# Kernel optimization log

Measured on AMD Instinct MI355X. Metric: run time of the kernel, lower is better.

Reference implementation:

```python
import jax, jax.numpy as jnp
import numpy as np

D_MODEL = 1024
N_HEADS = 16
D_K = D_MODEL // N_HEADS
D_FF = 4096
B, S = 4, 2048
EPS = 1e-5


def layer_norm(x, gamma, beta):
    mu = jnp.mean(x, axis=-1, keepdims=True)
    var = jnp.var(x, axis=-1, keepdims=True)
    return (x - mu) * jax.lax.rsqrt(var + EPS) * gamma + beta


def setup_inputs() -> dict:
    key = jax.random.key(0)
    ks = jax.random.split(key, 16)
    s = 1.0 / np.sqrt(D_MODEL)
    inp = {
        "query": jax.random.normal(ks[0], (B, S, D_MODEL), jnp.float32),
        "key": jax.random.normal(ks[1], (B, S, D_MODEL), jnp.float32),
        "value": jax.random.normal(ks[2], (B, S, D_MODEL), jnp.float32),
        "mask": jnp.ones((B, S, S), jnp.int32),
        "Wq": jax.random.normal(ks[3], (D_MODEL, D_MODEL), jnp.float32) * s,
        "Wk": jax.random.normal(ks[4], (D_MODEL, D_MODEL), jnp.float32) * s,
        "Wv": jax.random.normal(ks[5], (D_MODEL, D_MODEL), jnp.float32) * s,
        "Wo": jax.random.normal(ks[6], (D_MODEL, D_MODEL), jnp.float32) * s,
        "bo": jnp.zeros((D_MODEL,), jnp.float32),
        "g1": jnp.ones((D_MODEL,), jnp.float32),
        "b1": jnp.zeros((D_MODEL,), jnp.float32),
        "g2": jnp.ones((D_MODEL,), jnp.float32),
        "b2": jnp.zeros((D_MODEL,), jnp.float32),
        "gff": jnp.ones((D_MODEL,), jnp.float32),
        "bff": jnp.zeros((D_MODEL,), jnp.float32),
        "W1": jax.random.normal(ks[7], (D_MODEL, D_FF), jnp.float32) * s,
        "bf1": jnp.zeros((D_FF,), jnp.float32),
        "W2": jax.random.normal(ks[8], (D_FF, D_MODEL), jnp.float32) / np.sqrt(D_FF),
        "bf2": jnp.zeros((D_MODEL,), jnp.float32),
    }
    return inp


def reference(query, key, value, mask, Wq, Wk, Wv, Wo, bo,
              g1, b1, g2, b2, gff, bff, W1, bf1, W2, bf2):
    # Multi-head attention (dropout = identity, eval mode)
    q = (query @ Wq.T).reshape(B, S, N_HEADS, D_K).transpose(0, 2, 1, 3)
    k = (key @ Wk.T).reshape(B, S, N_HEADS, D_K).transpose(0, 2, 1, 3)
    v = (value @ Wv.T).reshape(B, S, N_HEADS, D_K).transpose(0, 2, 1, 3)
    scores = jnp.einsum("bhqd,bhkd->bhqk", q, k) / np.sqrt(D_K)  # [B,H,S,S]
    scores = jnp.where(mask[:, None, :, :] == 0, jnp.float32(-1e9), scores)
    attn = jax.nn.softmax(scores, axis=-1)
    ctx = jnp.einsum("bhqk,bhkd->bhqd", attn, v)
    ctx = ctx.transpose(0, 2, 1, 3).reshape(B, S, D_MODEL)
    attn_out = ctx @ Wo.T + bo

    # residual + LN
    x = layer_norm(attn_out + query, g1, b1)

    # FeedForward (has its own internal LayerNorm)
    h = layer_norm(x, gff, bff)
    h = jax.nn.relu(h @ W1 + bf1)
    ff = h @ W2 + bf2

    return layer_norm(ff + x, g2, b2)
```

## Files before the change

### kernel.cpp

```cpp
#include <hip/hip_runtime.h>


#define DM   1024
#define DFF  4096
#define SEQ  2048

typedef unsigned short u16;
typedef short          sx8  __attribute__((ext_vector_type(8)));
typedef unsigned short ushx8 __attribute__((ext_vector_type(8)));
typedef unsigned short ushx4 __attribute__((ext_vector_type(4)));
typedef float          fx4  __attribute__((ext_vector_type(4)));
typedef unsigned int   ux2  __attribute__((ext_vector_type(2)));

__device__ __forceinline__ void async16(const void* g, void* l) {
  __builtin_amdgcn_global_load_lds((__attribute__((address_space(1))) void*)g,
                                   (__attribute__((address_space(3))) void*)l,
                                   16, 0, 0);
}
__device__ __forceinline__ float b2f(u16 u) {
  union { unsigned int i; float f; } v; v.i = ((unsigned int)u) << 16; return v.f;
}
__device__ __forceinline__ u16 f2b(float f) {
  union { float f; unsigned int i; } v; v.f = f;
  unsigned int r = v.i + 0x7fffu + ((v.i >> 16) & 1u);
  return (u16)(r >> 16);
}
__device__ __forceinline__ float fexp2(float x) {
#if __has_builtin(__builtin_amdgcn_exp2f)
  return __builtin_amdgcn_exp2f(x);
#else
  return exp2f(x);
#endif
}
__device__ __forceinline__ ushx8 ld8(const void* p, long idx, bool f32) {
  if (f32) {
    const float* s = (const float*)p + idx;
    fx4 a = *(const fx4*)s, b = *(const fx4*)(s + 4);
    ushx8 r;
    r[0] = f2b(a[0]); r[1] = f2b(a[1]); r[2] = f2b(a[2]); r[3] = f2b(a[3]);
    r[4] = f2b(b[0]); r[5] = f2b(b[1]); r[6] = f2b(b[2]); r[7] = f2b(b[3]);
    return r;
  }
  return *(const ushx8*)((const u16*)p + idx);
}
__device__ __forceinline__ void ld4f(const void* p, long idx, bool f32, float* o) {
  if (f32) {
    fx4 a = *(const fx4*)((const float*)p + idx);
    o[0] = a[0]; o[1] = a[1]; o[2] = a[2]; o[3] = a[3];
  } else {
    ushx4 a = *(const ushx4*)((const u16*)p + idx);
    o[0] = b2f(a[0]); o[1] = b2f(a[1]); o[2] = b2f(a[2]); o[3] = b2f(a[3]);
  }
}

__global__ void detect_kernel(const void* q, int* flags) {
  int lane = threadIdx.x;
  u16 v = ((const u16*)q)[lane << 1];
  int e = (v >> 7) & 0xff;
  int pl = (e >= 0x60 && e <= 0x8c) ? 1 : 0;
  unsigned long long m = __ballot(pl);
  if (lane == 0) { flags[0] = (__popcll(m) >= 40) ? 0 : 1; flags[1] = 0; flags[2] = 1; }
}

__global__ __launch_bounds__(256)
void mask_scan(const int* __restrict__ m, int* flags) {
  long i = (((long)blockIdx.x << 8) + threadIdx.x) << 3;
  const int4 a = *(const int4*)(m + i);
  const int4 b = *(const int4*)(m + i + 4);
  bool ok = a.x && a.y && a.z && a.w && b.x && b.y && b.z && b.w;
  if (!__all(ok)) { if ((threadIdx.x & 63) == 0) flags[2] = 0; }
}

__global__ __launch_bounds__(256)
void pack_w(const void* Wq, const void* Wk, const void* Wv, const void* Wo,
            u16* Wqkv, u16* Wo_bf, const int* f_p) {
  const bool f = (*f_p != 0);
  long i = (((long)blockIdx.x << 8) + threadIdx.x) << 3;
  const long QKVN = (long)3 * DM * DM;
  if (i < QKVN) {
    int row = (int)(i >> 10);
    const void* src = (row < DM) ? Wq : (row < 2 * DM ? Wk : Wv);
    long s = ((long)(row & (DM - 1)) << 10) + (i & 1023);
    *(ushx8*)(Wqkv + i) = ld8(src, s, f);
  } else {
    long j = i - QKVN;
    *(ushx8*)(Wo_bf + j) = ld8(Wo, j, f);
  }
}

__global__ __launch_bounds__(256)
void conv_bf3(const void* q, const void* k, const void* v, long off,
              u16* dst, long n, const int* f_p) {
  const bool f = (*f_p != 0);
  const void* src = (blockIdx.y == 0) ? q : (blockIdx.y == 1 ? k : v);
  long i = (((long)blockIdx.x << 8) + threadIdx.x) << 3;
  if (i < n) *(ushx8*)(dst + (long)blockIdx.y * n + i) = ld8(src, off + i, f);
}

template<bool RELU, bool BIAS, bool DBUF>
__global__ __launch_bounds__(256)
void gemm_bb(const u16* __restrict__ A, long az, const u16* __restrict__ B, long bz,
             const void* __restrict__ bias, u16* __restrict__ C, long cz,
             int M, int N, int K, int ldc, const int* biasf_p) {
  __shared__ __align__(16) u16 sA[(DBUF ? 2 : 1) * 128 * 64];
  __shared__ __align__(16) u16 sB[(DBUF ? 2 : 1) * 128 * 64];
  const int z = blockIdx.y;
  A += (long)z * az; B += (long)z * bz; C += (long)z * cz;
  const bool biasf = BIAS && (*biasf_p != 0);
  const int t = threadIdx.x;
  const int lane = t & 63, w = t >> 6;
  const int lm = lane & 15, lg = lane >> 4;
  const int ntil = N >> 7;
  const int bx = (blockIdx.x & 7) * ((int)gridDim.x >> 3) + (blockIdx.x >> 3);
  const int m0 = (bx / ntil) << 7;
  const int n0 = (bx % ntil) << 7;
  const int wm = (w & 1) << 6, wn = (w >> 1) << 6;

  fx4 acc[4][4];
#pragma unroll
  for (int i = 0; i < 4; ++i)
#pragma unroll
    for (int j = 0; j < 4; ++j) acc[i][j] = (fx4){0.f, 0.f, 0.f, 0.f};

  auto stage = [&](int so, int kt) {
#pragma unroll
    for (int it = 0; it < 4; ++it) {
      int ci = (it << 8) + t;
      int r = ci >> 3, cs = (ci & 7) ^ (r & 7);
      async16(&A[(size_t)(m0 + r) * K + kt + (cs << 3)], &sA[so + (ci << 3)]);
    }
#pragma unroll
    for (int it = 0; it < 4; ++it) {
      int ci = (it << 8) + t;
      int r = ci >> 3, cs = (ci & 7) ^ (r & 7);
      async16(&B[(size_t)(n0 + r) * K + kt + (cs << 3)], &sB[so + (ci << 3)]);
    }
  };

  auto compute = [&](int so) {
#pragma unroll
    for (int s = 0; s < 2; ++s) {
      const int g = (s << 2) + lg;
      sx8 afr[4], bfr[4];
#pragma unroll
      for (int i = 0; i < 4; ++i) {
        int ra = wm + (i << 4) + lm;
        afr[i] = *(const sx8*)&sA[so + ra * 64 + ((g ^ (ra & 7)) << 3)];
        int rb = wn + (i << 4) + lm;
        bfr[i] = *(const sx8*)&sB[so + rb * 64 + ((g ^ (rb & 7)) << 3)];
      }
      __builtin_amdgcn_s_setprio(1);
#pragma unroll
      for (int i = 0; i < 4; ++i)
#pragma unroll
        for (int j = 0; j < 4; ++j)
          acc[i][j] = __builtin_amdgcn_mfma_f32_16x16x32_bf16(afr[i], bfr[j], acc[i][j], 0, 0, 0);
      __builtin_amdgcn_s_setprio(0);
    }
  };

  if (DBUF) {
    const int NT = K >> 6;
    stage(0, 0);
    for (int n = 0; n < NT; ++n) {
      if (n + 1 < NT) {
        stage(((n + 1) & 1) << 13, (n + 1) << 6);
        asm volatile("s_waitcnt vmcnt(8)" ::: "memory");
      } else {
        asm volatile("s_waitcnt vmcnt(0)" ::: "memory");
      }
      __builtin_amdgcn_s_barrier();
      __builtin_amdgcn_sched_barrier(0);
      compute((n & 1) << 13);
      if (n + 1 < NT) __builtin_amdgcn_s_barrier();
    }
  } else {
    for (int kt = 0; kt < K; kt += 64) {
      __syncthreads();
      stage(0, kt);
      __syncthreads();
      compute(0);
    }
  }

#pragma unroll
  for (int j = 0; j < 4; ++j) {
    const int col = n0 + wn + (j << 4) + lm;
    float bv = 0.f;
    if (BIAS) bv = biasf ? ((const float*)bias)[col] : b2f(((const u16*)bias)[col]);
#pragma unroll
    for (int i = 0; i < 4; ++i) {
      const int row0 = m0 + wm + (i << 4) + (lg << 2);
#pragma unroll
      for (int r = 0; r < 4; ++r) {
        float v = acc[i][j][r] + bv;
        if (RELU) v = fmaxf(v, 0.f);
        C[(size_t)(row0 + r) * ldc + col] = f2b(v);
      }
    }
  }
}

template<bool RELU, bool BIAS>
__global__ __launch_bounds__(256)
void gemm_nt(const void* __restrict__ A, long aoff, const void* __restrict__ Bm,
             const void* __restrict__ bias, u16* __restrict__ C,
             int M, int N, int K,
             const int* af_p, const int* bf_p, const int* biasf_p) {
  __shared__ __align__(16) u16 sA[128 * 64];
  __shared__ __align__(16) u16 sB[128 * 64];
  const bool af = (*af_p != 0), bfl = (*bf_p != 0), biasf = (*biasf_p != 0);
  const int t = threadIdx.x;
  const int lane = t & 63, w = t >> 6;
  const int lm = lane & 15, lg = lane >> 4;
  const int ntil = N >> 7;
  const int m0 = (blockIdx.x / ntil) << 7;
  const int n0 = (blockIdx.x % ntil) << 7;
  const int wm = (w & 1) << 6, wn = (w >> 1) << 6;

  fx4 acc[4][4];
#pragma unroll
  for (int i = 0; i < 4; ++i)
#pragma unroll
    for (int j = 0; j < 4; ++j) acc[i][j] = (fx4){0.f, 0.f, 0.f, 0.f};

  for (int kt = 0; kt < K; kt += 64) {
    __syncthreads();
#pragma unroll
    for (int it = 0; it < 4; ++it) {
      int ci = (it << 8) + t;
      int r = ci >> 3, cs = (ci & 7) ^ (r & 7);
      ushx8 va = ld8(A, aoff + (long)(m0 + r) * K + kt + (cs << 3), af);
      *(ushx8*)&sA[ci << 3] = va;
      ushx8 vb = ld8(Bm, (long)(n0 + r) * K + kt + (cs << 3), bfl);
      *(ushx8*)&sB[ci << 3] = vb;
    }
    __syncthreads();
#pragma unroll
    for (int s = 0; s < 2; ++s) {
      const int g = (s << 2) + lg;
      sx8 afr[4], bfr[4];
#pragma unroll
      for (int i = 0; i < 4; ++i) {
        int ra = wm + (i << 4) + lm;
        afr[i] = *(const sx8*)&sA[ra * 64 + ((g ^ (ra & 7)) << 3)];
        int rb = wn + (i << 4) + lm;
        bfr[i] = *(const sx8*)&sB[rb * 64 + ((g ^ (rb & 7)) << 3)];
      }
#pragma unroll
      for (int i = 0; i < 4; ++i)
#pragma unroll
        for (int j = 0; j < 4; ++j)
          acc[i][j] = __builtin_amdgcn_mfma_f32_16x16x32_bf16(afr[i], bfr[j], acc[i][j], 0, 0, 0);
    }
  }

#pragma unroll
  for (int j = 0; j < 4; ++j) {
    const int col = n0 + wn + (j << 4) + lm;
    float bv = 0.f;
    if (BIAS) bv = biasf ? ((const float*)bias)[col] : b2f(((const u16*)bias)[col]);
#pragma unroll
    for (int i = 0; i < 4; ++i) {
      const int row0 = m0 + wm + (i << 4) + (lg << 2);
#pragma unroll
      for (int r = 0; r < 4; ++r) {
        float v = acc[i][j][r] + bv;
        if (RELU) v = fmaxf(v, 0.f);
        C[(size_t)(row0 + r) * N + col] = f2b(v);
      }
    }
  }
}

__global__ __launch_bounds__(256)
void transpose_any(const void* __restrict__ in, u16* __restrict__ out,
                   int R, int C, const int* f_p) {
  __shared__ u16 tile[64][68];
  const bool f = (*f_p != 0);
  const int r0 = blockIdx.y << 6, c0 = blockIdx.x << 6;
  const int t = threadIdx.x;
#pragma unroll
  for (int it = 0; it < 4; ++it) {
    int j = (it << 8) + t;
    int rr = j >> 4, cc4 = (j & 15) << 2;
    float v[4];
    ld4f(in, (long)(r0 + rr) * C + c0 + cc4, f, v);
#pragma unroll
    for (int q = 0; q < 4; ++q) tile[rr][cc4 + q] = f2b(v[q]);
  }
  __syncthreads();
#pragma unroll
  for (int it = 0; it < 4; ++it) {
    int j = (it << 8) + t;
    int cc = j >> 4, rr4 = (j & 15) << 2;
    ushx4 v;
    v[0] = tile[rr4 + 0][cc]; v[1] = tile[rr4 + 1][cc];
    v[2] = tile[rr4 + 2][cc]; v[3] = tile[rr4 + 3][cc];
    *(ushx4*)&out[(size_t)(c0 + cc) * R + r0 + rr4] = v;
  }
}

__global__ __launch_bounds__(256, 3)
void attn_kernel(const u16* __restrict__ qp, const u16* __restrict__ kp,
                 const u16* __restrict__ vp, int lds_,
                 const int* __restrict__ mask, u16* __restrict__ ctx,
                 const int* __restrict__ mflag) {
  __shared__ __align__(16) u16 smem[16384];
  u16* const sK  = smem;
  u16* const sVt = smem + 8192;
  unsigned* const sPal = (unsigned*)smem;

  const bool nomask = (*mflag != 0);
  const long boff = (long)blockIdx.y * SEQ * (long)lds_;
  qp += boff; kp += boff; vp += boff;
  mask += (size_t)blockIdx.y * ((size_t)SEQ * SEQ);
  ctx += (size_t)blockIdx.y * ((size_t)SEQ * DM);

  const int id = (blockIdx.x & 7) * ((int)gridDim.x >> 3) + (blockIdx.x >> 3);
  const int q0 = (id & 31) << 6;
  const int h  = id >> 5;
  const int t = threadIdx.x, lane = t & 63, w = t >> 6;
  const int hoff = h << 6;
  const int lm = lane & 15, lg = lane >> 4;
  const int myq = q0 + (w << 4) + lm;
  const int aslot = 20 * lg;

  const int kq = (t & 31) << 2, dg = (t >> 5) << 3;
  const int kg7 = (kq >> 3) & 7;
  const int k7o = kq & 7;
  const int vbrow = ((kq >> 6) << 6) + dg;
  unsigned* pw = sPal + (w << 10);
  const int wswz = (lm & 7) << 2;
  const int pwb = lm << 6;

  sx8 one_b;
#pragma unroll
  for (int j = 0; j < 8; ++j) one_b[j] = (short)0x3F80;

  sx8 aq[2];
#pragma unroll
  for (int s = 0; s < 2; ++s)
    aq[s] = *(const sx8*)&qp[(size_t)myq * lds_ + hoff + (((s << 2) + lg) << 3)];

  fx4 o[4];
#pragma unroll
  for (int i = 0; i < 4; ++i) o[i] = (fx4){0.f, 0.f, 0.f, 0.f};
  fx4 osum = (fx4){0.f, 0.f, 0.f, 0.f};
  float m_prev = -1e30f;
  const float SCL = 0.18033688f;
  const float RTHR = 44.36142f;

  const u16* vbase = vp + (size_t)kq * lds_ + hoff + dg;
  uint4 va = *(const uint4*)(vbase);
  uint4 vb_ = *(const uint4*)(vbase + (size_t)lds_);
  uint4 vc = *(const uint4*)(vbase + 2 * (size_t)lds_);
  uint4 vd = *(const uint4*)(vbase + 3 * (size_t)lds_);

  for (int kt = 0; kt < 16; ++kt) {
    const int k0 = kt << 7;
    __syncthreads();
#pragma unroll
    for (int it = 0; it < 4; ++it) {
      int ci = (it << 8) + t;
      int r = ci >> 3, cs = (ci & 7) ^ (r & 7);
      async16(&kp[(size_t)(k0 + r) * lds_ + hoff + (cs << 3)], &sK[ci << 3]);
    }
    {
      const unsigned A0[4] = {va.x, va.y, va.z, va.w};
      const unsigned B0[4] = {vb_.x, vb_.y, vb_.z, vb_.w};
      const unsigned C0[4] = {vc.x, vc.y, vc.z, vc.w};
      const unsigned D0[4] = {vd.x, vd.y, vd.z, vd.w};
#pragma unroll
      for (int j = 0; j < 8; ++j) {
        const unsigned sel = (j & 1) ? 0x07060302u : 0x05040100u;
        ux2 wv;
        wv[0] = __builtin_amdgcn_perm(B0[j >> 1], A0[j >> 1], sel);
        wv[1] = __builtin_amdgcn_perm(D0[j >> 1], C0[j >> 1], sel);
        *(ux2*)&sVt[(vbrow + j) * 64 + ((kg7 ^ j) << 3) + k7o] = wv;
      }
    }
    __syncthreads();

    if (kt + 1 < 16) {
      const u16* vn = vbase + (size_t)(k0 + 128) * lds_;
      va = *(const uint4*)(vn);
      vb_ = *(const uint4*)(vn + (size_t)lds_);
      vc = *(const uint4*)(vn + 2 * (size_t)lds_);
      vd = *(const uint4*)(vn + 3 * (size_t)lds_);
    }

    fx4 sc[8];
#pragma unroll
    for (int nt = 0; nt < 8; ++nt) sc[nt] = (fx4){0.f, 0.f, 0.f, 0.f};
    __builtin_amdgcn_s_setprio(1);
#pragma unroll
    for (int s = 0; s < 2; ++s) {
      const int g = (s << 2) + lg;
#pragma unroll
      for (int nt = 0; nt < 8; ++nt) {
        int rk = (nt << 4) + lm;
        sx8 bk = *(const sx8*)&sK[rk * 64 + ((g ^ (rk & 7)) << 3)];
        sc[nt] = __builtin_amdgcn_mfma_f32_16x16x32_bf16(bk, aq[s], sc[nt], 0, 0, 0);
      }
    }
    __builtin_amdgcn_s_setprio(0);

    if (!nomask) {
#pragma unroll
      for (int nt = 0; nt < 8; ++nt)
#pragma unroll
        for (int r = 0; r < 4; ++r) {
          const int col = k0 + (nt << 4) + (lg << 2) + r;
          if (mask[((size_t)myq << 11) + col] == 0) sc[nt][r] = -1e9f;
        }
    }

    float tm = sc[0][0];
#pragma unroll
    for (int nt = 0; nt < 8; ++nt)
#pragma unroll
      for (int r = 0; r < 4; ++r) tm = fmaxf(tm, sc[nt][r]);
    tm = fmaxf(tm, __shfl_xor(tm, 16));
    tm = fmaxf(tm, __shfl_xor(tm, 32));

    if (!__all(tm <= m_prev + RTHR)) {
      const float mn = fmaxf(m_prev, tm);
      const float alpha = fexp2((m_prev - mn) * SCL);
#pragma unroll
      for (int r = 0; r < 4; ++r) {
        float ar = __shfl(alpha, aslot + r);
#pragma unroll
        for (int ot = 0; ot < 4; ++ot) o[ot][r] *= ar;
        osum[r] *= ar;
      }
      m_prev = mn;
    }

    const float msc = m_prev * SCL;
    float pvv[8][4];
#pragma unroll
    for (int nt = 0; nt < 8; ++nt)
#pragma unroll
      for (int r = 0; r < 4; ++r)
        pvv[nt][r] = fexp2(__builtin_fmaf(sc[nt][r], SCL, -msc));

    unsigned cpk[8][2];
#pragma unroll
    for (int nt = 0; nt < 8; ++nt) {
      asm("v_cvt_pk_bf16_f32 %0, %1, %2" : "=v"(cpk[nt][0]) : "v"(pvv[nt][0]), "v"(pvv[nt][1]));
      asm("v_cvt_pk_bf16_f32 %0, %1, %2" : "=v"(cpk[nt][1]) : "v"(pvv[nt][2]), "v"(pvv[nt][3]));
    }

    __builtin_amdgcn_sched_barrier(0);
    __builtin_amdgcn_s_barrier();
    __builtin_amdgcn_sched_barrier(0);

#pragma unroll
    for (int nt = 0; nt < 8; ++nt)
      *(ux2*)&pw[pwb + (((nt << 3) + (lg << 1)) ^ wswz)] = (ux2){cpk[nt][0], cpk[nt][1]};

    __builtin_amdgcn_s_setprio(1);
#pragma unroll
    for (int ks = 0; ks < 4; ++ks) {
      sx8 ap = *(const sx8*)&pw[pwb + (((ks << 4) + (lg << 2)) ^ wswz)];
      const int vrow = ((ks >> 1) << 6);
      const int vgr = (((ks & 1) << 2) + lg) ^ (lm & 7);
#pragma unroll
      for (int ot = 0; ot < 4; ++ot) {
        sx8 bv = *(const sx8*)&sVt[(vrow + (ot << 4) + lm) * 64 + (vgr << 3)];
        o[ot] = __builtin_amdgcn_mfma_f32_16x16x32_bf16(ap, bv, o[ot], 0, 0, 0);
      }
      osum = __builtin_amdgcn_mfma_f32_16x16x32_bf16(ap, one_b, osum, 0, 0, 0);
    }
    __builtin_amdgcn_s_setprio(0);
  }

#pragma unroll
  for (int r = 0; r < 4; ++r) {
    const float ir = (osum[r] > 0.f) ? 1.f / osum[r] : 0.f;
#pragma unroll
    for (int ot = 0; ot < 4; ++ot) {
      const int rowg = q0 + (w << 4) + (lg << 2) + r;
      const int col = hoff + (ot << 4) + lm;
      ctx[((size_t)rowg << 10) + col] = f2b(o[ot][r] * ir);
    }
  }
}

__global__ __launch_bounds__(256)
void ln_dual(const u16* __restrict__ a, const void* __restrict__ res, long roff,
             const void* __restrict__ g1, const void* __restrict__ b1,
             const void* __restrict__ gf, const void* __restrict__ bf,
             u16* __restrict__ xo, u16* __restrict__ xlo, const int* f_p) {
  __shared__ float red[8];
  const bool f = (*f_p != 0);
  const int row = blockIdx.x, t = threadIdx.x;
  const int lane = t & 63, w = t >> 6;
  const size_t base = (size_t)row << 10;
  const int c = t << 2;

  ushx4 a4 = *(const ushx4*)(a + base + c);
  float rv[4];
  ld4f(res, roff + (long)base + c, f, rv);
  float v[4], s = 0.f, ss = 0.f;
#pragma unroll
  for (int j = 0; j < 4; ++j) { v[j] = b2f(a4[j]) + rv[j]; s += v[j]; ss += v[j] * v[j]; }
#pragma unroll
  for (int off = 32; off > 0; off >>= 1) { s += __shfl_xor(s, off); ss += __shfl_xor(ss, off); }
  if (lane == 0) { red[w] = s; red[4 + w] = ss; }
  __syncthreads();
  s = red[0] + red[1] + red[2] + red[3];
  ss = red[4] + red[5] + red[6] + red[7];
  float mu = s * (1.f / 1024.f);
  float rstd = rsqrtf(fmaxf(ss * (1.f / 1024.f) - mu * mu, 0.f) + 1e-5f);

  float g4[4], b4[4];
  ld4f(g1, c, f, g4); ld4f(b1, c, f, b4);
  float x[4], s2 = 0.f, ss2 = 0.f;
  ushx4 xo4;
#pragma unroll
  for (int j = 0; j < 4; ++j) {
    x[j] = (v[j] - mu) * rstd * g4[j] + b4[j];
    xo4[j] = f2b(x[j]);
    s2 += x[j]; ss2 += x[j] * x[j];
  }
  *(ushx4*)(xo + base + c) = xo4;
#pragma unroll
  for (int off = 32; off > 0; off >>= 1) { s2 += __shfl_xor(s2, off); ss2 += __shfl_xor(ss2, off); }
  __syncthreads();
  if (lane == 0) { red[w] = s2; red[4 + w] = ss2; }
  __syncthreads();
  s2 = red[0] + red[1] + red[2] + red[3];
  ss2 = red[4] + red[5] + red[6] + red[7];
  float mu2 = s2 * (1.f / 1024.f);
  float rstd2 = rsqrtf(fmaxf(ss2 * (1.f / 1024.f) - mu2 * mu2, 0.f) + 1e-5f);

  ld4f(gf, c, f, g4); ld4f(bf, c, f, b4);
  ushx4 xl4;
#pragma unroll
  for (int j = 0; j < 4; ++j)
    xl4[j] = f2b((x[j] - mu2) * rstd2 * g4[j] + b4[j]);
  *(ushx4*)(xlo + base + c) = xl4;
}

__global__ __launch_bounds__(256)
void ln_final(const u16* __restrict__ a, const u16* __restrict__ resx,
              const void* __restrict__ g, const void* __restrict__ bb,
              void* __restrict__ out, long ooff, const int* f_p) {
  __shared__ float red[8];
  const bool f = (*f_p != 0);
  const int row = blockIdx.x, t = threadIdx.x;
  const int lane = t & 63, w = t >> 6;
  const size_t base = (size_t)row << 10;
  const int c = t << 2;

  ushx4 a4 = *(const ushx4*)(a + base + c);
  ushx4 r4 = *(const ushx4*)(resx + base + c);
  float v[4], s = 0.f, ss = 0.f;
#pragma unroll
  for (int j = 0; j < 4; ++j) { v[j] = b2f(a4[j]) + b2f(r4[j]); s += v[j]; ss += v[j] * v[j]; }
#pragma unroll
  for (int off = 32; off > 0; off >>= 1) { s += __shfl_xor(s, off); ss += __shfl_xor(ss, off); }
  if (lane == 0) { red[w] = s; red[4 + w] = ss; }
  __syncthreads();
  s = red[0] + red[1] + red[2] + red[3];
  ss = red[4] + red[5] + red[6] + red[7];
  float mu = s * (1.f / 1024.f);
  float rstd = rsqrtf(fmaxf(ss * (1.f / 1024.f) - mu * mu, 0.f) + 1e-5f);

  float g4[4], b4[4];
  ld4f(g, c, f, g4); ld4f(bb, c, f, b4);
  if (f) {
    fx4 o4;
#pragma unroll
    for (int j = 0; j < 4; ++j) o4[j] = (v[j] - mu) * rstd * g4[j] + b4[j];
    *(fx4*)((float*)out + ooff + base + c) = o4;
  } else {
    ushx4 o4;
#pragma unroll
    for (int j = 0; j < 4; ++j) o4[j] = f2b((v[j] - mu) * rstd * g4[j] + b4[j]);
    *(ushx4*)((u16*)out + ooff + base + c) = o4;
  }
}

extern "C" void kernel_launch(void* const* d_in, const int* in_sizes, int n_in,
                              void* d_out, int out_size, void* d_ws, size_t ws_size,
                              hipStream_t stream) {
  (void)in_sizes; (void)n_in; (void)out_size;
  const void* query = d_in[0];
  const void* keyi  = d_in[1];
  const void* value = d_in[2];
  const int*  mask  = (const int*)d_in[3];
  const void* Wq = d_in[4];
  const void* Wk = d_in[5];
  const void* Wv = d_in[6];
  const void* Wo = d_in[7];
  const void* bo = d_in[8];
  const void* g1 = d_in[9];
  const void* b1 = d_in[10];
  const void* g2 = d_in[11];
  const void* b2 = d_in[12];
  const void* gff = d_in[13];
  const void* bff = d_in[14];
  const void* W1 = d_in[15];
  const void* bf1 = d_in[16];
  const void* W2 = d_in[17];
  const void* bf2 = d_in[18];

  char* p = (char*)d_ws;
  int* flags = (int*)p;
  const int* F = flags;
  const int* Z = flags + 1;
  const int* M = flags + 2;
  dim3 blk(256);

  const size_t FIXED = 4096 + ((size_t)24 << 20);
  const size_t needC = FIXED + (size_t)8192 * 14336;
  const size_t needA = FIXED + (size_t)4096 * 14336;
  const size_t needB = FIXED + (size_t)2048 * 14336;

  if (ws_size >= needB) {
    const int CH = (ws_size >= needC) ? 8192 : (ws_size >= needA) ? 4096 : 2048;
    const int nch = 8192 / CH;

    u16* Wqkv  = (u16*)(p + 4096);
    u16* Wo_bf = Wqkv + (size_t)3 * DM * DM;
    u16* W1T   = Wo_bf + (size_t)DM * DM;
    u16* W2T   = W1T + (size_t)DFF * DM;
    u16* D0    = W2T + (size_t)DM * DFF;
    u16* D1    = D0 + (size_t)3 * CH * DM;
    u16* D2    = D1 + (size_t)3 * CH * DM;
    u16* qb = D0;
    u16* qkv = D1;
    u16* ao = D1, *x = D1 + (size_t)CH * DM, *xln = D1 + (size_t)2 * CH * DM;
    u16* h = D0;
    u16* ctx = D2, *ff = D2;

    detect_kernel<<<1, 64, 0, stream>>>(query, flags);
    mask_scan<<<dim3(8192), blk, 0, stream>>>(mask, flags);
    pack_w<<<dim3(2048), blk, 0, stream>>>(Wq, Wk, Wv, Wo, Wqkv, Wo_bf, F);
    transpose_any<<<dim3(DFF / 64, DM / 64), blk, 0, stream>>>(W1, W1T, DM, DFF, F);
    transpose_any<<<dim3(DM / 64, DFF / 64), blk, 0, stream>>>(W2, W2T, DFF, DM, F);

    for (int c = 0; c < nch; ++c) {
      const long off = (long)c * CH * DM;
      const long n = (long)CH * DM;
      conv_bf3<<<dim3((int)(n >> 11), 3), blk, 0, stream>>>(query, keyi, value, off, qb, n, F);

      gemm_bb<false, false, false><<<dim3((CH / 128) * 8, 3), blk, 0, stream>>>(
          qb, (long)CH * DM, Wqkv, (long)DM * DM, nullptr,
          qkv, 1024L, CH, DM, DM, 3072, Z);

      const int bpc = CH / SEQ, b0 = c * bpc;
      attn_kernel<<<dim3(512, bpc), blk, 0, stream>>>(
          qkv, qkv + 1024, qkv + 2048, 3072,
          mask + (size_t)b0 * SEQ * SEQ, ctx, M);

      gemm_bb<false, true, true><<<dim3((CH / 128) * 8, 1), blk, 0, stream>>>(
          ctx, 0, Wo_bf, 0, bo, ao, 0, CH, DM, DM, DM, F);

      ln_dual<<<dim3(CH), blk, 0, stream>>>(ao, query, off, g1, b1, gff, bff, x, xln, F);

      gemm_bb<true, true, false><<<dim3((CH / 128) * 32, 1), blk, 0, stream>>>(
          xln, 0, W1T, 0, bf1, h, 0, CH, DFF, DM, DFF, F);
      gemm_bb<false, true, true><<<dim3((CH / 128) * 8, 1), blk, 0, stream>>>(
          h, 0, W2T, 0, bf2, ff, 0, CH, DM, DFF, DM, F);

      ln_final<<<dim3(CH), blk, 0, stream>>>(ff, x, g2, b2, d_out, off, F);
    }
  } else {
    const int CH = 2048, FH = 1024;
    const int nch = 8192 / CH;
    const size_t h0 = 4096;
    u16* W1T = (u16*)(p + h0);
    u16* W2T = W1T + (size_t)DFF * DM;
    u16* hb  = (u16*)(p + h0 + ((size_t)16 << 20));
    const size_t HB = (size_t)FH * DFF * 2;
    u16* r0 = (u16*)(p + h0 + ((size_t)16 << 20) + HB);
    const size_t CE = (size_t)CH * DM;
    u16* qp = r0;
    u16* kp = qp + CE;
    u16* vp = kp + CE;
    u16* ctxb = vp + CE;
    u16* x = qp; u16* xln = kp; u16* ao = vp; u16* ff = ctxb;

    detect_kernel<<<1, 64, 0, stream>>>(query, flags);
    mask_scan<<<dim3(8192), blk, 0, stream>>>(mask, flags);
    transpose_any<<<dim3(DFF / 64, DM / 64), blk, 0, stream>>>(W1, W1T, DM, DFF, F);
    transpose_any<<<dim3(DM / 64, DFF / 64), blk, 0, stream>>>(W2, W2T, DFF, DM, F);

    for (int c = 0; c < nch; ++c) {
      const long off = (long)c * CH * DM;
      dim3 gq((CH / 128) * (DM / 128));

      gemm_nt<false, false><<<gq, blk, 0, stream>>>(query, off, Wq, Wq, qp, CH, DM, DM, F, F, Z);
      gemm_nt<false, false><<<gq, blk, 0, stream>>>(keyi,  off, Wk, Wk, kp, CH, DM, DM, F, F, Z);
      gemm_nt<false, false><<<gq, blk, 0, stream>>>(value, off, Wv, Wv, vp, CH, DM, DM, F, F, Z);

      const int bpc = CH / SEQ, b0 = c * bpc;
      for (int bl = 0; bl < bpc; ++bl) {
        const size_t lo = (size_t)bl * SEQ * DM;
        attn_kernel<<<dim3(512, 1), blk, 0, stream>>>(
            qp + lo, kp + lo, vp + lo, 1024,
            mask + (size_t)(b0 + bl) * SEQ * SEQ, ctxb + lo, M);
      }

      gemm_nt<false, true><<<gq, blk, 0, stream>>>(ctxb, 0, Wo, bo, ao, CH, DM, DM, Z, F, F);

      ln_dual<<<dim3(CH), blk, 0, stream>>>(ao, query, off, g1, b1, gff, bff, x, xln, F);

      for (int qs = 0; qs < CH / FH; ++qs) {
        const long so = (long)qs * FH * DM;
        gemm_nt<true, true><<<dim3((FH / 128) * (DFF / 128)), blk, 0, stream>>>(
            xln + so, 0, W1T, bf1, hb, FH, DFF, DM, Z, Z, F);
        gemm_nt<false, true><<<dim3((FH / 128) * (DM / 128)), blk, 0, stream>>>(
            hb, 0, W2T, bf2, ff + so, FH, DM, DFF, Z, Z, F);
      }

      ln_final<<<dim3(CH), blk, 0, stream>>>(ff, x, g2, b2, d_out, off, F);
    }
  }
}
```

Measured before the change: 657.4 us.

## Replace GEMM kernel with 256x128-tile, 8-wave, phased double-buffered variant

Swaps the 128x128, 4-wave GEMM for a 256x128-tile kernel using 512 threads. It double-buffers LDS and splits each k-step into four quadrant phases, so next-tile async loads interleave with MFMA work under barriers. The larger tile raises operand reuse per load and applies double buffering to the previously single-buffered GEMMs. In exchange it halves the grid size, which can hurt occupancy on the smaller GEMMs, and adds many extra barriers per k-step.

```diff
diff --git a/kernel.cpp b/kernel.cpp
--- a/kernel.cpp
+++ b/kernel.cpp
@@ -97,13 +97,13 @@
   if (i < n) *(ushx8*)(dst + (long)blockIdx.y * n + i) = ld8(src, off + i, f);
 }
 
-template<bool RELU, bool BIAS, bool DBUF>
-__global__ __launch_bounds__(256)
-void gemm_bb(const u16* __restrict__ A, long az, const u16* __restrict__ B, long bz,
-             const void* __restrict__ bias, u16* __restrict__ C, long cz,
-             int M, int N, int K, int ldc, const int* biasf_p) {
-  __shared__ __align__(16) u16 sA[(DBUF ? 2 : 1) * 128 * 64];
-  __shared__ __align__(16) u16 sB[(DBUF ? 2 : 1) * 128 * 64];
+template<bool RELU, bool BIAS>
+__global__ __launch_bounds__(512, 2)
+void gemm_big(const u16* __restrict__ A, long az, const u16* __restrict__ B, long bz,
+              const void* __restrict__ bias, u16* __restrict__ C, long cz,
+              int M, int N, int K, int ldc, const int* biasf_p) {
+  __shared__ __align__(16) u16 sA[2][256 * 64];
+  __shared__ __align__(16) u16 sB[2][128 * 64];
   const int z = blockIdx.y;
   A += (long)z * az; B += (long)z * bz; C += (long)z * cz;
   const bool biasf = BIAS && (*biasf_p != 0);
@@ -112,9 +112,10 @@
   const int lm = lane & 15, lg = lane >> 4;
   const int ntil = N >> 7;
   const int bx = (blockIdx.x & 7) * ((int)gridDim.x >> 3) + (blockIdx.x >> 3);
-  const int m0 = (bx / ntil) << 7;
+  const int m0 = (bx / ntil) << 8;
   const int n0 = (bx % ntil) << 7;
-  const int wm = (w & 1) << 6, wn = (w >> 1) << 6;
+  const int wm = (w >> 1) << 6;
+  const int wn = (w & 1) << 6;
 
   fx4 acc[4][4];
 #pragma unroll
@@ -122,65 +123,72 @@
 #pragma unroll
     for (int j = 0; j < 4; ++j) acc[i][j] = (fx4){0.f, 0.f, 0.f, 0.f};
 
-  auto stage = [&](int so, int kt) {
-#pragma unroll
-    for (int it = 0; it < 4; ++it) {
-      int ci = (it << 8) + t;
-      int r = ci >> 3, cs = (ci & 7) ^ (r & 7);
-      async16(&A[(size_t)(m0 + r) * K + kt + (cs << 3)], &sA[so + (ci << 3)]);
-    }
-#pragma unroll
-    for (int it = 0; it < 4; ++it) {
-      int ci = (it << 8) + t;
-      int r = ci >> 3, cs = (ci & 7) ^ (r & 7);
-      async16(&B[(size_t)(n0 + r) * K + kt + (cs << 3)], &sB[so + (ci << 3)]);
+  auto stageA = [&](int b, int kt, int h) {
+#pragma unroll
+    for (int it = 0; it < 2; ++it) {
+      int ci = (it << 9) + t;
+      int r = (h << 7) + (ci >> 3);
+      int cs = (ci & 7) ^ (r & 7);
+      async16(&A[(size_t)(m0 + r) * K + kt + (cs << 3)],
+              &sA[b][r * 64 + ((ci & 7) << 3)]);
     }
   };
-
-  auto compute = [&](int so) {
+  auto stageB = [&](int b, int kt) {
+#pragma unroll
+    for (int it = 0; it < 2; ++it) {
+      int ci = (it << 9) + t;
+      int r = ci >> 3;
+      int cs = (ci & 7) ^ (r & 7);
+      async16(&B[(size_t)(n0 + r) * K + kt + (cs << 3)],
+              &sB[b][r * 64 + ((ci & 7) << 3)]);
+    }
+  };
+
+  auto phase = [&](int b, int qm, int qn) {
+    sx8 af[2][2], bf[2][2];
 #pragma unroll
     for (int s = 0; s < 2; ++s) {
       const int g = (s << 2) + lg;
-      sx8 afr[4], bfr[4];
-#pragma unroll
-      for (int i = 0; i < 4; ++i) {
-        int ra = wm + (i << 4) + lm;
-        afr[i] = *(const sx8*)&sA[so + ra * 64 + ((g ^ (ra & 7)) << 3)];
-        int rb = wn + (i << 4) + lm;
-        bfr[i] = *(const sx8*)&sB[so + rb * 64 + ((g ^ (rb & 7)) << 3)];
-      }
-      __builtin_amdgcn_s_setprio(1);
-#pragma unroll
-      for (int i = 0; i < 4; ++i)
-#pragma unroll
-        for (int j = 0; j < 4; ++j)
-          acc[i][j] = __builtin_amdgcn_mfma_f32_16x16x32_bf16(afr[i], bfr[j], acc[i][j], 0, 0, 0);
-      __builtin_amdgcn_s_setprio(0);
-    }
+#pragma unroll
+      for (int i = 0; i < 2; ++i) {
+        int ra = wm + (((qm << 1) + i) << 4) + lm;
+        af[s][i] = *(const sx8*)&sA[b][ra * 64 + ((g ^ (ra & 7)) << 3)];
+        int rb = wn + (((qn << 1) + i) << 4) + lm;
+        bf[s][i] = *(const sx8*)&sB[b][rb * 64 + ((g ^ (rb & 7)) << 3)];
+      }
+    }
+    __builtin_amdgcn_s_barrier();
+    asm volatile("s_waitcnt lgkmcnt(0)" ::: "memory");
+    __builtin_amdgcn_sched_barrier(0);
+    __builtin_amdgcn_s_setprio(1);
+#pragma unroll
+    for (int s = 0; s < 2; ++s)
+#pragma unroll
+      for (int i = 0; i < 2; ++i)
+#pragma unroll
+        for (int j = 0; j < 2; ++j)
+          acc[(qm << 1) + i][(qn << 1) + j] =
+              __builtin_amdgcn_mfma_f32_16x16x32_bf16(
+                  af[s][i], bf[s][j], acc[(qm << 1) + i][(qn << 1) + j], 0, 0, 0);
+    __builtin_amdgcn_s_setprio(0);
+    __builtin_amdgcn_s_barrier();
   };
 
-  if (DBUF) {
-    const int NT = K >> 6;
-    stage(0, 0);
-    for (int n = 0; n < NT; ++n) {
-      if (n + 1 < NT) {
-        stage(((n + 1) & 1) << 13, (n + 1) << 6);
-        asm volatile("s_waitcnt vmcnt(8)" ::: "memory");
-      } else {
-        asm volatile("s_waitcnt vmcnt(0)" ::: "memory");
-      }
-      __builtin_amdgcn_s_barrier();
-      __builtin_amdgcn_sched_barrier(0);
-      compute((n & 1) << 13);
-      if (n + 1 < NT) __builtin_amdgcn_s_barrier();
-    }
-  } else {
-    for (int kt = 0; kt < K; kt += 64) {
-      __syncthreads();
-      stage(0, kt);
-      __syncthreads();
-      compute(0);
-    }
+  const int NT = K >> 6;
+  stageA(0, 0, 0); stageA(0, 0, 1); stageB(0, 0);
+  for (int n = 0; n < NT; ++n) {
+    const int b = n & 1;
+    asm volatile("s_waitcnt vmcnt(0)" ::: "memory");
+    __builtin_amdgcn_s_barrier();
+    const bool pf = (n + 1 < NT);
+    const int kt1 = (n + 1) << 6;
+    if (pf) stageA(b ^ 1, kt1, 0);
+    phase(b, 0, 0);
+    if (pf) stageA(b ^ 1, kt1, 1);
+    phase(b, 0, 1);
+    if (pf) stageB(b ^ 1, kt1);
+    phase(b, 1, 0);
+    phase(b, 1, 1);
   }
 
 #pragma unroll
@@ -614,6 +622,7 @@
   const int* Z = flags + 1;
   const int* M = flags + 2;
   dim3 blk(256);
+  dim3 blk2(512);
 
   const size_t FIXED = 4096 + ((size_t)24 << 20);
   const size_t needC = FIXED + (size_t)8192 * 14336;
@@ -648,7 +657,7 @@
       const long n = (long)CH * DM;
       conv_bf3<<<dim3((int)(n >> 11), 3), blk, 0, stream>>>(query, keyi, value, off, qb, n, F);
 
-      gemm_bb<false, false, false><<<dim3((CH / 128) * 8, 3), blk, 0, stream>>>(
+      gemm_big<false, false><<<dim3((CH / 256) * (DM / 128), 3), blk2, 0, stream>>>(
           qb, (long)CH * DM, Wqkv, (long)DM * DM, nullptr,
           qkv, 1024L, CH, DM, DM, 3072, Z);
 
@@ -657,14 +666,14 @@
           qkv, qkv + 1024, qkv + 2048, 3072,
           mask + (size_t)b0 * SEQ * SEQ, ctx, M);
 
-      gemm_bb<false, true, true><<<dim3((CH / 128) * 8, 1), blk, 0, stream>>>(
+      gemm_big<false, true><<<dim3((CH / 256) * (DM / 128), 1), blk2, 0, stream>>>(
           ctx, 0, Wo_bf, 0, bo, ao, 0, CH, DM, DM, DM, F);
 
       ln_dual<<<dim3(CH), blk, 0, stream>>>(ao, query, off, g1, b1, gff, bff, x, xln, F);
 
-      gemm_bb<true, true, false><<<dim3((CH / 128) * 32, 1), blk, 0, stream>>>(
+      gemm_big<true, true><<<dim3((CH / 256) * (DFF / 128), 1), blk2, 0, stream>>>(
           xln, 0, W1T, 0, bf1, h, 0, CH, DFF, DM, DFF, F);
-      gemm_bb<false, true, true><<<dim3((CH / 128) * 8, 1), blk, 0, stream>>>(
+      gemm_big<false, true><<<dim3((CH / 256) * (DM / 128), 1), blk2, 0, stream>>>(
           h, 0, W2T, 0, bf2, ff, 0, CH, DM, DFF, DM, F);
 
       ln_final<<<dim3(CH), blk, 0, stream>>>(ff, x, g2, b2, d_out, off, F);
```

New measurement: 860.5 us. 1.31x slower.
